# Kernel optimization log

Measured on AMD Instinct MI355X. Metric: run time of the kernel, lower is better.

Reference implementation:

```python
import jax, jax.numpy as jnp
import numpy as np

C_M, C_Z, N_HEADS = 256, 128, 8
HEAD_DIM = C_M // N_HEADS
EPS = 1e-5


def _layer_norm(x, scale, bias):
    mu = jnp.mean(x, axis=-1, keepdims=True)
    var = jnp.mean(jnp.square(x - mu), axis=-1, keepdims=True)
    return (x - mu) * jax.lax.rsqrt(var + EPS) * scale + bias


def setup_inputs() -> dict:
    key = jax.random.key(0)
    ks = jax.random.split(key, 12)
    N, L = 128, 256
    s_m = 1.0 / np.sqrt(C_M)
    s_z = 1.0 / np.sqrt(C_Z)
    return {
        "msa": jax.random.normal(ks[0], (N, L, C_M), dtype=jnp.float32),
        "pair": jax.random.normal(ks[1], (L, L, C_Z), dtype=jnp.float32),
        "ln_m_scale": jnp.ones((C_M,), jnp.float32),
        "ln_m_bias": jnp.zeros((C_M,), jnp.float32),
        "ln_z_scale": jnp.ones((C_Z,), jnp.float32),
        "ln_z_bias": jnp.zeros((C_Z,), jnp.float32),
        "w_q": jax.random.normal(ks[2], (C_M, C_M), jnp.float32) * s_m,
        "w_k": jax.random.normal(ks[3], (C_M, C_M), jnp.float32) * s_m,
        "w_v": jax.random.normal(ks[4], (C_M, C_M), jnp.float32) * s_m,
        "w_b": jax.random.normal(ks[5], (N_HEADS, C_Z), jnp.float32) * s_z,
        "w_out": jax.random.normal(ks[6], (C_M, C_M), jnp.float32) * s_m,
        "b_out": jnp.zeros((C_M,), jnp.float32),
        "w_gate": jax.random.normal(ks[7], (C_M, C_M), jnp.float32) * s_m,
        "b_gate": jnp.zeros((C_M,), jnp.float32),
    }


def reference(msa, pair, ln_m_scale, ln_m_bias, ln_z_scale, ln_z_bias,
              w_q, w_k, w_v, w_b, w_out, b_out, w_gate, b_gate):
    N, L, _ = msa.shape
    m = _layer_norm(msa, ln_m_scale, ln_m_bias)          # (N, L, c_m)
    z = _layer_norm(pair, ln_z_scale, ln_z_bias)         # (L, L, c_z)
    q = (m @ w_q.T).reshape(N, L, N_HEADS, HEAD_DIM)
    k = (m @ w_k.T).reshape(N, L, N_HEADS, HEAD_DIM)
    v = (m @ w_v.T).reshape(N, L, N_HEADS, HEAD_DIM)
    attn = jnp.einsum('bihd,bjhd->bhij', q, k) / np.sqrt(HEAD_DIM).astype(np.float32)
    bias = jnp.einsum('ijc,hc->hij', z, w_b)             # (H, L, L)
    attn = jax.nn.softmax(attn + bias[None], axis=-1)    # (N, H, L, L)
    out = jnp.einsum('bhij,bjhd->bihd', attn, v).reshape(N, L, C_M)
    return msa + jax.nn.sigmoid(m @ w_gate.T + b_gate) * (out @ w_out.T + b_out)
```

## Files before the change

kernel.cpp:

```cpp
#include <hip/hip_runtime.h>

typedef unsigned short u16;
typedef float f32x4 __attribute__((ext_vector_type(4)));
typedef __bf16 bf16x8 __attribute__((ext_vector_type(8)));

__device__ __forceinline__ u16 f2bf(float f) {
  union { float f; unsigned u; } v; v.f = f;
  unsigned r = (v.u + 0x7fffu + ((v.u >> 16) & 1u)) >> 16;
  return (u16)r;
}
__device__ __forceinline__ float bf2f(u16 h) {
  union { unsigned u; float f; } v; v.u = ((unsigned)h) << 16; return v.f;
}

#define GLOAD16(gp, lp)                                                        \
  __builtin_amdgcn_global_load_lds(                                            \
      (const __attribute__((address_space(1))) void*)(gp),                     \
      (__attribute__((address_space(3))) void*)(lp), 16, 0, 0)

#define LOG2E 1.4426950408889634f
#define HS 1048576

__global__ __launch_bounds__(256) void pre_kernel(
    const float* __restrict__ x, const float* __restrict__ sc,
    const float* __restrict__ bi, u16* __restrict__ mo,
    const float* __restrict__ wq, const float* __restrict__ wk,
    const float* __restrict__ wv, const float* __restrict__ wg,
    const float* __restrict__ wo, u16* __restrict__ wcat, u16* __restrict__ wobf)
{
  if (blockIdx.x < 8192) {
    const int row  = blockIdx.x * 4 + (threadIdx.x >> 6);
    const int lane = threadIdx.x & 63;
    const float4 v = *(const float4*)(x + (size_t)row * 256 + lane * 4);
    float s = v.x + v.y + v.z + v.w;
    #pragma unroll
    for (int off = 1; off < 64; off <<= 1) s += __shfl_xor(s, off);
    const float mu = s * 0.00390625f;
    const float d0 = v.x - mu, d1 = v.y - mu, d2 = v.z - mu, d3 = v.w - mu;
    float vs = d0*d0 + d1*d1 + d2*d2 + d3*d3;
    #pragma unroll
    for (int off = 1; off < 64; off <<= 1) vs += __shfl_xor(vs, off);
    const float rstd = rsqrtf(vs * 0.00390625f + 1e-5f);
    const float4 scv = *(const float4*)(sc + lane * 4);
    const float4 biv = *(const float4*)(bi + lane * 4);
    ushort4 o;
    o.x = f2bf(d0 * rstd * scv.x + biv.x);
    o.y = f2bf(d1 * rstd * scv.y + biv.y);
    o.z = f2bf(d2 * rstd * scv.z + biv.z);
    o.w = f2bf(d3 * rstd * scv.w + biv.w);
    *(ushort4*)(mo + (size_t)row * 256 + lane * 4) = o;
  } else {
    int idx = (blockIdx.x - 8192) * 256 + threadIdx.x;
    int e = idx * 4;
    int row = e >> 8;
    int col = e & 255;
    const float* src = (row < 256)  ? (wq + (size_t)row * 256)
                     : (row < 512)  ? (wk + (size_t)(row - 256) * 256)
                     : (row < 768)  ? (wv + (size_t)(row - 512) * 256)
                     : (row < 1024) ? (wg + (size_t)(row - 768) * 256)
                                    : (wo + (size_t)(row - 1024) * 256);
    float4 v = *(const float4*)(src + col);
    ushort4 o;
    o.x = f2bf(v.x); o.y = f2bf(v.y); o.z = f2bf(v.z); o.w = f2bf(v.w);
    if (row < 1024) *(ushort4*)(wcat + e) = o;
    else            *(ushort4*)(wobf + (e - 262144)) = o;
  }
}

__global__ __launch_bounds__(256) void ln_pair_fast(
    const float* __restrict__ pair, const float* __restrict__ sc,
    const float* __restrict__ bi, const float* __restrict__ wb,
    u16* __restrict__ biasQ)
{
  __shared__ float swc[1024];
  __shared__ float sA[8], sB2[8];
  const int tid = threadIdx.x;
  #pragma unroll
  for (int k = 0; k < 4; ++k) {
    int idx = k * 256 + tid;
    int c = idx >> 3, h = idx & 7;
    swc[idx] = sc[c] * wb[h * 128 + c];
  }
  __syncthreads();
  if (tid < 8) {
    float a = 0.f, b2 = 0.f;
    for (int c = 0; c < 128; ++c) {
      a  += swc[c * 8 + tid];
      b2 += bi[c] * wb[tid * 128 + c];
    }
    sA[tid] = a; sB2[tid] = b2;
  }
  __syncthreads();

  const int gt = blockIdx.x * 256 + tid;
  const int ij = gt >> 1, hg = gt & 1;
  const float* xr = pair + (size_t)ij * 128;
  float s = 0.f, ss = 0.f;
  float d0 = 0.f, d1 = 0.f, d2 = 0.f, d3 = 0.f;
  for (int c0 = 0; c0 < 128; c0 += 4) {
    float4 xv4 = *(const float4*)(xr + c0);
    float xe[4] = {xv4.x, xv4.y, xv4.z, xv4.w};
    #pragma unroll
    for (int e = 0; e < 4; ++e) {
      const float xv = xe[e];
      s += xv; ss += xv * xv;
      const f32x4 wv = *(const f32x4*)&swc[(c0 + e) * 8 + hg * 4];
      d0 += xv * wv[0]; d1 += xv * wv[1];
      d2 += xv * wv[2]; d3 += xv * wv[3];
    }
  }
  const float mu = s * 0.0078125f;
  const float rstd = rsqrtf(ss * 0.0078125f - mu * mu + 1e-5f);
  const int i = ij >> 8, j = ij & 255;
  const float dd[4] = {d0, d1, d2, d3};
  #pragma unroll
  for (int hh = 0; hh < 4; ++hh) {
    const int h = hg * 4 + hh;
    const float bias = (dd[hh] - mu * sA[h]) * rstd + sB2[h];
    biasQ[h * 65536 + i * 256 + j] = f2bf(bias * LOG2E);
  }
}

template<int EPI, int NCG>
__global__ __launch_bounds__(256, 4) void gemm_bstat(
    const u16* __restrict__ A, const u16* __restrict__ B,
    u16* __restrict__ qh, u16* __restrict__ kh, u16* __restrict__ vh,
    u16* __restrict__ gateb, const float* __restrict__ bgate,
    float* __restrict__ Cf, const float* __restrict__ msa,
    const float* __restrict__ bout)
{
  __shared__ u16 sB[64 * 256];
  const int tid = threadIdx.x, lane = tid & 63, w = tid >> 6;
  const int g = lane >> 4, r15 = lane & 15;
  const int x = blockIdx.x & 7;
  const int j = blockIdx.x >> 3;
  const int cg = j % NCG;
  const int rpl = j / NCG;
  const int bcol = cg * 64;

  #pragma unroll
  for (int i = 0; i < 8; ++i) {
    int c = i * 256 + tid;
    int col = c >> 5, s = c & 31;
    int lc = (s & 24) | ((s ^ col) & 7);
    GLOAD16(B + (size_t)(bcol + col) * 256 + lc * 8, &sB[c * 8]);
  }

  float gb[4] = {0.f, 0.f, 0.f, 0.f};
  if (EPI == 0 && cg >= (NCG * 3) / 4) {
    #pragma unroll
    for (int n = 0; n < 4; ++n) gb[n] = bgate[bcol - 768 + n * 16 + r15];
  }
  float bo[4] = {0.f, 0.f, 0.f, 0.f};
  if (EPI == 1) {
    #pragma unroll
    for (int n = 0; n < 4; ++n) bo[n] = bout[bcol + n * 16 + r15];
  }

  const size_t brow = ((size_t)(x * 32) + rpl) * 128;
  bf16x8 af[2][8];
  #pragma unroll
  for (int m = 0; m < 2; ++m) {
    const size_t arow = brow + w * 32 + m * 16 + r15;
    #pragma unroll
    for (int kk = 0; kk < 8; ++kk)
      af[m][kk] = *(const bf16x8*)(A + arow * 256 + kk * 32 + g * 8);
  }
  __syncthreads();

  f32x4 acc[2][4] = {};
  #pragma unroll
  for (int kk = 0; kk < 8; ++kk) {
    bf16x8 bfr[4];
    #pragma unroll
    for (int n = 0; n < 4; ++n) {
      int col = n * 16 + r15;
      int lcq = kk * 4 + g;
      int s = (lcq & 24) | ((lcq ^ col) & 7);
      bfr[n] = *(const bf16x8*)&sB[col * 256 + s * 8];
    }
    #pragma unroll
    for (int m = 0; m < 2; ++m)
      #pragma unroll
      for (int n = 0; n < 4; ++n)
        acc[m][n] = __builtin_amdgcn_mfma_f32_16x16x32_bf16(af[m][kk], bfr[n], acc[m][n], 0, 0, 0);
  }

  #pragma unroll
  for (int m = 0; m < 2; ++m) {
    const int row0 = (int)brow + w * 32 + m * 16 + g * 4;
    #pragma unroll
    for (int n = 0; n < 4; ++n) {
      const int col = bcol + n * 16 + r15;
      #pragma unroll
      for (int rr = 0; rr < 4; ++rr) {
        float v = acc[m][n][rr];
        const size_t orow = (size_t)(row0 + rr);
        if (EPI == 0) {
          if (col < 256) {
            v *= 0.17677669529663687f * LOG2E;
            qh[(size_t)(col >> 5) * HS + orow * 32 + (col & 31)] = f2bf(v);
          } else if (col < 512) {
            const int c = col - 256;
            kh[(size_t)(c >> 5) * HS + orow * 32 + (c & 31)] = f2bf(v);
          } else if (col < 768) {
            const int c = col - 512;
            vh[(size_t)(c >> 5) * HS + orow * 32 + (c & 31)] = f2bf(v);
          } else {
            v = 1.0f / (1.0f + __expf(-(v + gb[n])));
            gateb[orow * 256 + (col - 768)] = f2bf(v);
          }
        } else {
          v += bo[n];
          float gg = bf2f(gateb[orow * 256 + col]);
          Cf[orow * 256 + col] = msa[orow * 256 + col] + gg * v;
        }
      }
    }
  }
}

__global__ __launch_bounds__(256) void attn_kernel(
    const u16* __restrict__ qh, const u16* __restrict__ kh,
    const u16* __restrict__ vh, const u16* __restrict__ biasQ,
    u16* __restrict__ attn_out)
{
  __shared__ u16 sVt[32 * 264];
  const int blk = blockIdx.x;
  const int h = blk & 7;
  const int idx2 = blk >> 3;
  const int qh_i = idx2 & 1;
  const int b = idx2 >> 1;
  const int tid = threadIdx.x, lane = tid & 63, w = tid >> 6;
  const int g = lane >> 4, r15 = lane & 15;
  const size_t rowbase = (size_t)b * 256;
  const int qbase = qh_i * 128;

  const u16* Qh = qh + (size_t)h * HS;
  const u16* Kh = kh + (size_t)h * HS;
  const u16* Vh = vh + (size_t)h * HS;

  {
    const int nl = (tid >> 4) & 3, q4 = tid & 15;
    const int pos = (tid >> 6) * 64 + (nl >> 1) * 32 + (q4 >> 2) * 8 + (nl & 1) * 4 + (q4 & 3);
    const uint4* vr4 = (const uint4*)(Vh + (rowbase + tid) * 32);
    #pragma unroll
    for (int c = 0; c < 4; ++c) {
      uint4 vv = vr4[c];
      unsigned uu[4] = {vv.x, vv.y, vv.z, vv.w};
      #pragma unroll
      for (int p = 0; p < 4; ++p) {
        sVt[(c * 8 + p * 2    ) * 264 + pos] = (u16)(uu[p] & 0xffffu);
        sVt[(c * 8 + p * 2 + 1) * 264 + pos] = (u16)(uu[p] >> 16);
      }
    }
  }

  const int qrel0 = qbase + w * 32 + r15;
  bf16x8 qf[2];
  #pragma unroll
  for (int m = 0; m < 2; ++m)
    qf[m] = *(const bf16x8*)(Qh + (rowbase + qrel0 + m * 16) * 32 + g * 8);
  __syncthreads();

  f32x4 oacc[2][2] = {};
  float lrun[2] = {0.f, 0.f};
  const u16* biasH = biasQ + (size_t)h * 65536;

  bf16x8 kf[4];
  ushort4 bvu[2][4];
  #pragma unroll
  for (int n = 0; n < 4; ++n)
    kf[n] = *(const bf16x8*)(Kh + (rowbase + n * 16 + r15) * 32 + g * 8);
  #pragma unroll
  for (int m = 0; m < 2; ++m)
    #pragma unroll
    for (int n = 0; n < 4; ++n)
      bvu[m][n] = *(const ushort4*)(biasH + (size_t)(qrel0 + m * 16) * 256 + n * 16 + g * 4);

  for (int jb = 0; jb < 4; ++jb) {
    f32x4 s[2][4];
    #pragma unroll
    for (int m = 0; m < 2; ++m) {
      #pragma unroll
      for (int n = 0; n < 4; ++n) {
        f32x4 z = {0.f, 0.f, 0.f, 0.f};
        s[m][n] = __builtin_amdgcn_mfma_f32_16x16x32_bf16(kf[n], qf[m], z, 0, 0, 0);
        const u16* bb = (const u16*)&bvu[m][n];
        #pragma unroll
        for (int rr = 0; rr < 4; ++rr) s[m][n][rr] += bf2f(bb[rr]);
      }
    }
    if (jb < 3) {
      const int j1 = jb + 1;
      #pragma unroll
      for (int n = 0; n < 4; ++n)
        kf[n] = *(const bf16x8*)(Kh + (rowbase + j1 * 64 + n * 16 + r15) * 32 + g * 8);
      #pragma unroll
      for (int m = 0; m < 2; ++m)
        #pragma unroll
        for (int n = 0; n < 4; ++n)
          bvu[m][n] = *(const ushort4*)(biasH + (size_t)(qrel0 + m * 16) * 256 + j1 * 64 + n * 16 + g * 4);
    }
    #pragma unroll
    for (int m = 0; m < 2; ++m)
      #pragma unroll
      for (int n = 0; n < 4; ++n)
        #pragma unroll
        for (int rr = 0; rr < 4; ++rr) {
          float p = __builtin_amdgcn_exp2f(s[m][n][rr]);
          s[m][n][rr] = p;
          lrun[m] += p;
        }
    #pragma unroll
    for (int kb = 0; kb < 2; ++kb) {
      bf16x8 vt[2];
      #pragma unroll
      for (int nd = 0; nd < 2; ++nd)
        vt[nd] = *(const bf16x8*)&sVt[(nd * 16 + r15) * 264 + jb * 64 + kb * 32 + g * 8];
      #pragma unroll
      for (int m = 0; m < 2; ++m) {
        bf16x8 pv;
        #pragma unroll
        for (int rr = 0; rr < 4; ++rr) {
          pv[rr]     = (__bf16)s[m][2 * kb][rr];
          pv[4 + rr] = (__bf16)s[m][2 * kb + 1][rr];
        }
        #pragma unroll
        for (int nd = 0; nd < 2; ++nd)
          oacc[m][nd] = __builtin_amdgcn_mfma_f32_16x16x32_bf16(pv, vt[nd], oacc[m][nd], 0, 0, 0);
      }
    }
  }

  #pragma unroll
  for (int m = 0; m < 2; ++m) {
    float l = lrun[m];
    l += __shfl_xor(l, 16);
    l += __shfl_xor(l, 32);
    const float inv = 1.0f / l;
    #pragma unroll
    for (int rr = 0; rr < 4; ++rr) {
      const float invq = __shfl(inv, g * 4 + rr);
      const size_t qrow = rowbase + qbase + w * 32 + m * 16 + g * 4 + rr;
      #pragma unroll
      for (int nd = 0; nd < 2; ++nd)
        attn_out[qrow * 256 + h * 32 + nd * 16 + r15] = f2bf(oacc[m][nd][rr] * invq);
    }
  }
}

extern "C" void kernel_launch(void* const* d_in, const int* in_sizes, int n_in,
                              void* d_out, int out_size, void* d_ws, size_t ws_size,
                              hipStream_t stream)
{
  (void)in_sizes; (void)n_in; (void)out_size; (void)ws_size;
  const float* msa        = (const float*)d_in[0];
  const float* pair       = (const float*)d_in[1];
  const float* ln_m_scale = (const float*)d_in[2];
  const float* ln_m_bias  = (const float*)d_in[3];
  const float* ln_z_scale = (const float*)d_in[4];
  const float* ln_z_bias  = (const float*)d_in[5];
  const float* w_q        = (const float*)d_in[6];
  const float* w_k        = (const float*)d_in[7];
  const float* w_v        = (const float*)d_in[8];
  const float* w_b        = (const float*)d_in[9];
  const float* w_out      = (const float*)d_in[10];
  const float* b_out      = (const float*)d_in[11];
  const float* w_gate     = (const float*)d_in[12];
  const float* b_gate     = (const float*)d_in[13];

  char* ws = (char*)d_ws;
  u16*   m_bf   = (u16*)(ws);
  u16*   wcat   = (u16*)(ws + 16777216);
  u16*   wobf   = (u16*)(ws + 17301504);
  u16*   qh     = (u16*)(ws + 17432576);
  u16*   kh     = (u16*)(ws + 34209792);
  u16*   vh     = (u16*)(ws + 50987008);
  u16*   gateb  = (u16*)(ws + 67764224);
  u16*   biasQ  = (u16*)(ws + 84541440);
  u16*   attn_o = (u16*)(ws + 86638592);
  float* out = (float*)d_out;

  pre_kernel<<<dim3(8512), dim3(256), 0, stream>>>(
      msa, ln_m_scale, ln_m_bias, m_bf, w_q, w_k, w_v, w_gate, w_out, wcat, wobf);
  ln_pair_fast<<<dim3(512), dim3(256), 0, stream>>>(
      pair, ln_z_scale, ln_z_bias, w_b, biasQ);
  gemm_bstat<0, 16><<<dim3(4096), dim3(256), 0, stream>>>(m_bf, wcat, qh, kh, vh, gateb,
                                                          b_gate, nullptr, nullptr, nullptr);
  attn_kernel<<<dim3(2048), dim3(256), 0, stream>>>(qh, kh, vh, biasQ, attn_o);
  gemm_bstat<1, 4><<<dim3(1024), dim3(256), 0, stream>>>(attn_o, wobf, nullptr, nullptr, nullptr,
                                                         gateb, nullptr, out, msa, b_out);
}
```

Baseline: 138.7 us.

## Merge pair layernorm into pre kernel and stage QKV-gate epilogue through LDS

The pair-layernorm bias computation moves into the pre_kernel as extra blocks, which removes one kernel launch and lets that work overlap with the msa layernorm and weight conversion. The QKV/gate GEMM epilogue now writes bf16 results into shared memory (reusing sB with a padded stride of 72) and then stores them as coalesced 16-byte vectors to the head-major q/k/v and gate buffers, replacing scattered 2-byte global stores. The per-block branch on column group replaces the per-element column checks. The cost is an extra pair of barriers, LDS traffic in the epilogue, and a larger shared-memory footprint in pre_kernel for all blocks.

```diff
diff --git a/kernel.cpp b/kernel.cpp
--- a/kernel.cpp
+++ b/kernel.cpp
@@ -26,11 +26,18 @@
     const float* __restrict__ bi, u16* __restrict__ mo,
     const float* __restrict__ wq, const float* __restrict__ wk,
     const float* __restrict__ wv, const float* __restrict__ wg,
-    const float* __restrict__ wo, u16* __restrict__ wcat, u16* __restrict__ wobf)
+    const float* __restrict__ wo, u16* __restrict__ wcat, u16* __restrict__ wobf,
+    const float* __restrict__ pair, const float* __restrict__ scz,
+    const float* __restrict__ biz, const float* __restrict__ wb,
+    u16* __restrict__ biasQ)
 {
+  __shared__ float swc[1024];
+  __shared__ float sA[8], sB2[8];
+  const int tid = threadIdx.x;
+
   if (blockIdx.x < 8192) {
-    const int row  = blockIdx.x * 4 + (threadIdx.x >> 6);
-    const int lane = threadIdx.x & 63;
+    const int row  = blockIdx.x * 4 + (tid >> 6);
+    const int lane = tid & 63;
     const float4 v = *(const float4*)(x + (size_t)row * 256 + lane * 4);
     float s = v.x + v.y + v.z + v.w;
     #pragma unroll
@@ -49,8 +56,8 @@
     o.z = f2bf(d2 * rstd * scv.z + biv.z);
     o.w = f2bf(d3 * rstd * scv.w + biv.w);
     *(ushort4*)(mo + (size_t)row * 256 + lane * 4) = o;
-  } else {
-    int idx = (blockIdx.x - 8192) * 256 + threadIdx.x;
+  } else if (blockIdx.x < 8512) {
+    int idx = (blockIdx.x - 8192) * 256 + tid;
     int e = idx * 4;
     int row = e >> 8;
     int col = e & 255;
@@ -64,60 +71,50 @@
     o.x = f2bf(v.x); o.y = f2bf(v.y); o.z = f2bf(v.z); o.w = f2bf(v.w);
     if (row < 1024) *(ushort4*)(wcat + e) = o;
     else            *(ushort4*)(wobf + (e - 262144)) = o;
-  }
-}
-
-__global__ __launch_bounds__(256) void ln_pair_fast(
-    const float* __restrict__ pair, const float* __restrict__ sc,
-    const float* __restrict__ bi, const float* __restrict__ wb,
-    u16* __restrict__ biasQ)
-{
-  __shared__ float swc[1024];
-  __shared__ float sA[8], sB2[8];
-  const int tid = threadIdx.x;
-  #pragma unroll
-  for (int k = 0; k < 4; ++k) {
-    int idx = k * 256 + tid;
-    int c = idx >> 3, h = idx & 7;
-    swc[idx] = sc[c] * wb[h * 128 + c];
-  }
-  __syncthreads();
-  if (tid < 8) {
-    float a = 0.f, b2 = 0.f;
-    for (int c = 0; c < 128; ++c) {
-      a  += swc[c * 8 + tid];
-      b2 += bi[c] * wb[tid * 128 + c];
-    }
-    sA[tid] = a; sB2[tid] = b2;
-  }
-  __syncthreads();
-
-  const int gt = blockIdx.x * 256 + tid;
-  const int ij = gt >> 1, hg = gt & 1;
-  const float* xr = pair + (size_t)ij * 128;
-  float s = 0.f, ss = 0.f;
-  float d0 = 0.f, d1 = 0.f, d2 = 0.f, d3 = 0.f;
-  for (int c0 = 0; c0 < 128; c0 += 4) {
-    float4 xv4 = *(const float4*)(xr + c0);
-    float xe[4] = {xv4.x, xv4.y, xv4.z, xv4.w};
-    #pragma unroll
-    for (int e = 0; e < 4; ++e) {
-      const float xv = xe[e];
-      s += xv; ss += xv * xv;
-      const f32x4 wv = *(const f32x4*)&swc[(c0 + e) * 8 + hg * 4];
-      d0 += xv * wv[0]; d1 += xv * wv[1];
-      d2 += xv * wv[2]; d3 += xv * wv[3];
-    }
-  }
-  const float mu = s * 0.0078125f;
-  const float rstd = rsqrtf(ss * 0.0078125f - mu * mu + 1e-5f);
-  const int i = ij >> 8, j = ij & 255;
-  const float dd[4] = {d0, d1, d2, d3};
-  #pragma unroll
-  for (int hh = 0; hh < 4; ++hh) {
-    const int h = hg * 4 + hh;
-    const float bias = (dd[hh] - mu * sA[h]) * rstd + sB2[h];
-    biasQ[h * 65536 + i * 256 + j] = f2bf(bias * LOG2E);
+  } else {
+    #pragma unroll
+    for (int k = 0; k < 4; ++k) {
+      int idx = k * 256 + tid;
+      int c = idx >> 3, h = idx & 7;
+      swc[idx] = scz[c] * wb[h * 128 + c];
+    }
+    __syncthreads();
+    if (tid < 8) {
+      float a = 0.f, b2 = 0.f;
+      for (int c = 0; c < 128; ++c) {
+        a  += swc[c * 8 + tid];
+        b2 += biz[c] * wb[tid * 128 + c];
+      }
+      sA[tid] = a; sB2[tid] = b2;
+    }
+    __syncthreads();
+    const int gt = (blockIdx.x - 8512) * 256 + tid;
+    const int ij = gt >> 1, hg = gt & 1;
+    const float* xr = pair + (size_t)ij * 128;
+    float s = 0.f, ss = 0.f;
+    float d0 = 0.f, d1 = 0.f, d2 = 0.f, d3 = 0.f;
+    for (int c0 = 0; c0 < 128; c0 += 4) {
+      float4 xv4 = *(const float4*)(xr + c0);
+      float xe[4] = {xv4.x, xv4.y, xv4.z, xv4.w};
+      #pragma unroll
+      for (int e = 0; e < 4; ++e) {
+        const float xv = xe[e];
+        s += xv; ss += xv * xv;
+        const f32x4 wv = *(const f32x4*)&swc[(c0 + e) * 8 + hg * 4];
+        d0 += xv * wv[0]; d1 += xv * wv[1];
+        d2 += xv * wv[2]; d3 += xv * wv[3];
+      }
+    }
+    const float mu = s * 0.0078125f;
+    const float rstd = rsqrtf(ss * 0.0078125f - mu * mu + 1e-5f);
+    const int i = ij >> 8, j = ij & 255;
+    const float dd[4] = {d0, d1, d2, d3};
+    #pragma unroll
+    for (int hh = 0; hh < 4; ++hh) {
+      const int h = hg * 4 + hh;
+      const float bias = (dd[hh] - mu * sA[h]) * rstd + sB2[h];
+      biasQ[h * 65536 + i * 256 + j] = f2bf(bias * LOG2E);
+    }
   }
 }
 
@@ -186,32 +183,55 @@
         acc[m][n] = __builtin_amdgcn_mfma_f32_16x16x32_bf16(af[m][kk], bfr[n], acc[m][n], 0, 0, 0);
   }
 
-  #pragma unroll
-  for (int m = 0; m < 2; ++m) {
-    const int row0 = (int)brow + w * 32 + m * 16 + g * 4;
-    #pragma unroll
-    for (int n = 0; n < 4; ++n) {
-      const int col = bcol + n * 16 + r15;
-      #pragma unroll
-      for (int rr = 0; rr < 4; ++rr) {
-        float v = acc[m][n][rr];
-        const size_t orow = (size_t)(row0 + rr);
-        if (EPI == 0) {
-          if (col < 256) {
-            v *= 0.17677669529663687f * LOG2E;
-            qh[(size_t)(col >> 5) * HS + orow * 32 + (col & 31)] = f2bf(v);
-          } else if (col < 512) {
-            const int c = col - 256;
-            kh[(size_t)(c >> 5) * HS + orow * 32 + (c & 31)] = f2bf(v);
-          } else if (col < 768) {
-            const int c = col - 512;
-            vh[(size_t)(c >> 5) * HS + orow * 32 + (c & 31)] = f2bf(v);
-          } else {
+  if (EPI == 0) {
+    __syncthreads();
+    #pragma unroll
+    for (int m = 0; m < 2; ++m) {
+      const int lr0 = w * 32 + m * 16 + g * 4;
+      #pragma unroll
+      for (int n = 0; n < 4; ++n) {
+        const int colL = n * 16 + r15;
+        #pragma unroll
+        for (int rr = 0; rr < 4; ++rr) {
+          float v = acc[m][n][rr];
+          if (cg < NCG / 4) v *= 0.17677669529663687f * LOG2E;
+          else if (cg >= (NCG * 3) / 4)
             v = 1.0f / (1.0f + __expf(-(v + gb[n])));
-            gateb[orow * 256 + (col - 768)] = f2bf(v);
-          }
-        } else {
-          v += bo[n];
+          sB[(lr0 + rr) * 72 + colL] = f2bf(v);
+        }
+      }
+    }
+    __syncthreads();
+    #pragma unroll
+    for (int i = 0; i < 4; ++i) {
+      const int c = i * 256 + tid;
+      const int lr = c >> 3, cc = (c & 7) * 8;
+      const size_t rowg = brow + lr;
+      const uint4 vv = *(const uint4*)&sB[lr * 72 + cc];
+      const int colg = bcol + cc;
+      if (cg < NCG / 4) {
+        *(uint4*)(qh + (size_t)(colg >> 5) * HS + rowg * 32 + (colg & 31)) = vv;
+      } else if (cg < NCG / 2) {
+        const int c2 = colg - 256;
+        *(uint4*)(kh + (size_t)(c2 >> 5) * HS + rowg * 32 + (c2 & 31)) = vv;
+      } else if (cg < (NCG * 3) / 4) {
+        const int c2 = colg - 512;
+        *(uint4*)(vh + (size_t)(c2 >> 5) * HS + rowg * 32 + (c2 & 31)) = vv;
+      } else {
+        *(uint4*)(gateb + rowg * 256 + (colg - 768)) = vv;
+      }
+    }
+  } else {
+    #pragma unroll
+    for (int m = 0; m < 2; ++m) {
+      const int row0 = (int)brow + w * 32 + m * 16 + g * 4;
+      #pragma unroll
+      for (int n = 0; n < 4; ++n) {
+        const int col = bcol + n * 16 + r15;
+        #pragma unroll
+        for (int rr = 0; rr < 4; ++rr) {
+          float v = acc[m][n][rr] + bo[n];
+          const size_t orow = (size_t)(row0 + rr);
           float gg = bf2f(gateb[orow * 256 + col]);
           Cf[orow * 256 + col] = msa[orow * 256 + col] + gg * v;
         }
@@ -382,9 +402,8 @@
   u16*   attn_o = (u16*)(ws + 86638592);
   float* out = (float*)d_out;
 
-  pre_kernel<<<dim3(8512), dim3(256), 0, stream>>>(
-      msa, ln_m_scale, ln_m_bias, m_bf, w_q, w_k, w_v, w_gate, w_out, wcat, wobf);
-  ln_pair_fast<<<dim3(512), dim3(256), 0, stream>>>(
+  pre_kernel<<<dim3(9024), dim3(256), 0, stream>>>(
+      msa, ln_m_scale, ln_m_bias, m_bf, w_q, w_k, w_v, w_gate, w_out, wcat, wobf,
       pair, ln_z_scale, ln_z_bias, w_b, biasQ);
   gemm_bstat<0, 16><<<dim3(4096), dim3(256), 0, stream>>>(m_bf, wcat, qh, kh, vh, gateb,
                                                           b_gate, nullptr, nullptr, nullptr);
```

Result: no change. 141.1 us (+1.8%).
